# Optimization experiments

Measured on AMD Instinct MI355X. Metric: run time of the kernel, lower is better.

Reference implementation:

```python
import jax, jax.numpy as jnp
import numpy as np

N_HEAD = 16
MAX_SEQ_LEN = 2048
RATIO = 1
NEG_INF = -jnp.inf


def make_alibi_bias(n_head: int, max_seq_len: int, ratio: int) -> jnp.ndarray:
    # bias[t, s] = s*ratio - t, masked to -inf where > 0 (future positions)
    s = jnp.arange(max_seq_len)[None, :] * ratio            # [1, S]
    t = jnp.arange(max_seq_len * ratio)[:, None]            # [T, 1]
    bias = (s - t).astype(jnp.float32)                      # [T, S]
    bias = jnp.where(bias > 0, NEG_INF, bias)
    # per-head slopes: cumprod of 2^(-8/n_head) -> m_i = 2^(-8*(i+1)/n_head)
    m = jnp.cumprod(jnp.full((n_head,), 2.0 ** (-8.0 / n_head), dtype=jnp.float32))
    return bias[None, :, :] * m[:, None, None]              # [H, T, S]


def setup_inputs() -> dict:
    key = jax.random.key(0)
    kq, kk, kv = jax.random.split(key, 3)
    B, T, D = 2, 2048, 1024
    return {
        "q": jax.random.normal(kq, (B, T, D), dtype=jnp.float32),
        "k": jax.random.normal(kk, (B, T, D), dtype=jnp.float32),
        "v": jax.random.normal(kv, (B, T, D), dtype=jnp.float32),
    }


def reference(q, k, v):
    B, T, D = q.shape
    S = k.shape[1]
    H = N_HEAD
    dh = D // H
    # split heads: [B, T, D] -> [B, H, T, dh]
    qh = q.reshape(B, T, H, dh).transpose(0, 2, 1, 3)
    kh = k.reshape(B, S, H, dh).transpose(0, 2, 1, 3)
    vh = v.reshape(B, S, H, dh).transpose(0, 2, 1, 3)

    scores = jnp.einsum("bhtd,bhsd->bhts", qh, kh) / jnp.sqrt(jnp.float32(dh))
    bias = make_alibi_bias(H, MAX_SEQ_LEN, RATIO)[:, -T:, -S:]  # [H, T, S]
    attn = jax.nn.softmax(scores + bias[None], axis=-1)
    out = jnp.einsum("bhts,bhsd->bhtd", attn, vh)
    # gather heads: [B, H, T, dh] -> [B, T, D]
    return out.transpose(0, 2, 1, 3).reshape(B, T, D)
```

## Files before the change

### kernel.cpp

```cpp
#include <hip/hip_runtime.h>

#define N_HEAD 16
#define DHEAD 64
#define TSEQ 2048
#define DMODEL 1024
#define BATCH 2

typedef __bf16 bf16x8 __attribute__((ext_vector_type(8)));
typedef float f32x4 __attribute__((ext_vector_type(4)));

union BF8 { bf16x8 v; uint4 u; unsigned short us[8]; };

#if __has_builtin(__builtin_amdgcn_exp2f)
#define EXP2F(x) __builtin_amdgcn_exp2f(x)
#else
#define EXP2F(x) exp2f(x)
#endif

__device__ __forceinline__ unsigned short f2bf(float f) {
    unsigned u = __float_as_uint(f);
    u += 0x7fffu + ((u >> 16) & 1u);
    return (unsigned short)(u >> 16);
}

__device__ __forceinline__ bf16x8 load_bf8_f32(const float* p) {
    const float4 f0 = *(const float4*)p;
    const float4 f1 = *(const float4*)(p + 4);
    BF8 r;
    r.us[0] = f2bf(f0.x); r.us[1] = f2bf(f0.y);
    r.us[2] = f2bf(f0.z); r.us[3] = f2bf(f0.w);
    r.us[4] = f2bf(f1.x); r.us[5] = f2bf(f1.y);
    r.us[6] = f2bf(f1.z); r.us[7] = f2bf(f1.w);
    return r.v;
}

__global__ __launch_bounds__(256) void prep(const float* __restrict__ K,
                                            const float* __restrict__ V,
                                            unsigned short* __restrict__ Kp,
                                            unsigned short* __restrict__ Vt)
{
    __shared__ float tl[64][68];
    const int bh = blockIdx.y, b = bh >> 4, h = bh & 15;
    const int s0 = blockIdx.x * 64;
    const int t = threadIdx.x;
    const int r16 = t >> 4, c4 = (t & 15) * 4;
    #pragma unroll
    for (int pass = 0; pass < 4; ++pass) {
        const int row = pass * 16 + r16;
        const size_t goff = ((size_t)(b * TSEQ + s0 + row)) * DMODEL + h * DHEAD + c4;
        const float4 fk = *(const float4*)(K + goff);
        ushort4 ok;
        ok.x = f2bf(fk.x); ok.y = f2bf(fk.y); ok.z = f2bf(fk.z); ok.w = f2bf(fk.w);
        *(ushort4*)(Kp + (((size_t)bh * TSEQ + s0 + row) << 6) + c4) = ok;
        const float4 fv = *(const float4*)(V + goff);
        *(float4*)&tl[row][c4] = fv;
    }
    __syncthreads();
    const int d = t >> 2, sc = (t & 3) * 16;
    union { unsigned short us[8]; uint4 u; } pk0, pk1;
    #pragma unroll
    for (int j = 0; j < 8; ++j) pk0.us[j] = f2bf(tl[sc + j][d]);
    #pragma unroll
    for (int j = 0; j < 8; ++j) pk1.us[j] = f2bf(tl[sc + 8 + j][d]);
    unsigned short* vo = Vt + ((size_t)bh * DHEAD + d) * TSEQ + s0 + sc;
    *(uint4*)vo = pk0.u;
    *(uint4*)(vo + 8) = pk1.u;
}

struct KF { uint4 f[8]; };

__global__ __launch_bounds__(256, 2) void alibi_attn(
    const float* __restrict__ Q, const unsigned short* __restrict__ Kp,
    const unsigned short* __restrict__ Vt, float* __restrict__ O)
{
    __shared__ __align__(16) unsigned short p_lds[4][32][72];
    __shared__ __align__(16) float mlds[2][64][40];

    const int wave = threadIdx.x >> 6;
    const int lane = threadIdx.x & 63;
    const int quad = lane >> 4;
    const int l16  = lane & 15;
    const int rh   = wave & 1;
    const int par  = wave >> 1;

    const int bh = blockIdx.y;
    const int b  = bh >> 4;
    const int h  = bh & 15;

    const float LOG2E   = 1.44269504088896f;
    const float slope   = exp2f(-0.5f * (float)(h + 1));
    const float bslope2 = slope * LOG2E;
    const float sscale2 = 0.125f * LOG2E;
    const float step128 = 128.0f * bslope2;

    const float*          qp = Q  + (size_t)b * TSEQ * DMODEL + (size_t)h * DHEAD;
    const unsigned short* kp = Kp + (size_t)bh * TSEQ * DHEAD;
    const unsigned short* vp = Vt + (size_t)bh * DHEAD * TSEQ;

    const f32x4 zero4 = {0.f, 0.f, 0.f, 0.f};

    for (int half = 0; half < 2; ++half) {
        const int x   = half ? (31 - (int)blockIdx.x) : (int)blockIdx.x;
        const int q0b = x * 64;
        const int qrow_base = q0b + rh * 32;

        if (half) __syncthreads();

        bf16x8 aq[2][2];
        #pragma unroll
        for (int qs = 0; qs < 2; ++qs) {
            const float* qr = qp + (size_t)(qrow_base + qs * 16 + l16) * DMODEL + quad * 8;
            aq[qs][0] = load_bf8_f32(qr);
            aq[qs][1] = load_bf8_f32(qr + 32);
        }

        f32x4 o[2][4], lp[2], dd[2][4];
        #pragma unroll
        for (int qs = 0; qs < 2; ++qs) {
            lp[qs] = zero4;
            #pragma unroll
            for (int nt = 0; nt < 4; ++nt) o[qs][nt] = zero4;
        }
        const int kvs = 64 * par;
        #pragma unroll
        for (int qs = 0; qs < 2; ++qs)
            #pragma unroll
            for (int nt = 0; nt < 4; ++nt) {
                const int d0 = kvs + nt * 16 + l16 - (qrow_base + qs * 16 + quad * 4);
                f32x4 dv = {(float)d0, (float)(d0 - 1), (float)(d0 - 2), (float)(d0 - 3)};
                dd[qs][nt] = dv * bslope2;
            }

        auto loadK = [&](int t) {
            KF f;
            const unsigned short* kb = kp + ((size_t)(t * 64 + l16) << 6) + quad * 8;
            #pragma unroll
            for (int nt = 0; nt < 4; ++nt) {
                f.f[nt * 2 + 0] = *(const uint4*)(kb + nt * 1024);
                f.f[nt * 2 + 1] = *(const uint4*)(kb + nt * 1024 + 32);
            }
            return f;
        };

        auto compute = [&](const KF& kf, int t, bool masked) {
            const int kv0 = t * 64;
            uint4 vf[4][2];
            #pragma unroll
            for (int nt = 0; nt < 4; ++nt)
                #pragma unroll
                for (int ks = 0; ks < 2; ++ks)
                    vf[nt][ks] = *(const uint4*)(vp + (size_t)(nt * 16 + l16) * TSEQ +
                                                 kv0 + ks * 32 + quad * 8);
            f32x4 s[2][4];
            #pragma unroll
            for (int qs = 0; qs < 2; ++qs)
                #pragma unroll
                for (int nt = 0; nt < 4; ++nt) {
                    BF8 k0, k1;
                    k0.u = kf.f[nt * 2 + 0];
                    k1.u = kf.f[nt * 2 + 1];
                    f32x4 acc = zero4;
                    acc = __builtin_amdgcn_mfma_f32_16x16x32_bf16(aq[qs][0], k0.v, acc, 0, 0, 0);
                    acc = __builtin_amdgcn_mfma_f32_16x16x32_bf16(aq[qs][1], k1.v, acc, 0, 0, 0);
                    s[qs][nt] = acc;
                }
            #pragma unroll
            for (int qs = 0; qs < 2; ++qs)
                #pragma unroll
                for (int nt = 0; nt < 4; ++nt) {
                    f32x4 e = s[qs][nt] * sscale2 + dd[qs][nt];
                    f32x4 p;
                    if (!masked) {
                        #pragma unroll
                        for (int r = 0; r < 4; ++r) p[r] = EXP2F(e[r]);
                    } else {
                        const int db = kv0 + nt * 16 + l16 - (qrow_base + qs * 16 + quad * 4);
                        #pragma unroll
                        for (int r = 0; r < 4; ++r) {
                            const float v = EXP2F(e[r]);
                            p[r] = (db - r > 0) ? 0.f : v;
                        }
                    }
                    lp[qs] += p;
                    #pragma unroll
                    for (int r = 0; r < 4; ++r)
                        p_lds[wave][qs * 16 + quad * 4 + r][nt * 16 + l16] =
                            (unsigned short)(__float_as_uint(p[r]) >> 16);
                    dd[qs][nt] += step128;
                }
            asm volatile("s_waitcnt lgkmcnt(0)" ::: "memory");
            BF8 pa[2][2];
            #pragma unroll
            for (int qs = 0; qs < 2; ++qs)
                #pragma unroll
                for (int ks = 0; ks < 2; ++ks)
                    pa[qs][ks].u = *(const uint4*)&p_lds[wave][qs * 16 + l16][ks * 32 + quad * 8];
            #pragma unroll
            for (int qs = 0; qs < 2; ++qs)
                #pragma unroll
                for (int nt = 0; nt < 4; ++nt) {
                    BF8 v0, v1;
                    v0.u = vf[nt][0];
                    v1.u = vf[nt][1];
                    o[qs][nt] = __builtin_amdgcn_mfma_f32_16x16x32_bf16(pa[qs][0].v, v0.v, o[qs][nt], 0, 0, 0);
                    o[qs][nt] = __builtin_amdgcn_mfma_f32_16x16x32_bf16(pa[qs][1].v, v1.v, o[qs][nt], 0, 0, 0);
                }
        };

        if (par <= x) {
            int t = par;
            KF A = loadK(t);
            for (; t + 2 < x; t += 4) {
                KF B = loadK(t + 2);
                compute(A, t, false);
                const int tn = (t + 4 < x) ? (t + 4) : x;
                A = loadK(tn);
                compute(B, t + 2, false);
            }
            if (t == x) {
                compute(A, t, true);
            } else if (t == x - 1) {
                compute(A, t, false);
            } else if (t == x - 2) {
                KF B2 = loadK(x);
                compute(A, t, false);
                compute(B2, x, true);
            }
        }

        if (par == 1) {
            float* m = &mlds[rh][lane][0];
            #pragma unroll
            for (int qs = 0; qs < 2; ++qs)
                #pragma unroll
                for (int nt = 0; nt < 4; ++nt)
                    *(f32x4*)&m[(qs * 4 + nt) * 4] = o[qs][nt];
            *(f32x4*)&m[32] = lp[0];
            *(f32x4*)&m[36] = lp[1];
        }
        __syncthreads();
        if (par == 0) {
            const float* m = &mlds[rh][lane][0];
            #pragma unroll
            for (int qs = 0; qs < 2; ++qs)
                #pragma unroll
                for (int nt = 0; nt < 4; ++nt)
                    o[qs][nt] += *(const f32x4*)&m[(qs * 4 + nt) * 4];
            lp[0] += *(const f32x4*)&m[32];
            lp[1] += *(const f32x4*)&m[36];
            float ls[2][4];
            #pragma unroll
            for (int qs = 0; qs < 2; ++qs)
                #pragma unroll
                for (int r = 0; r < 4; ++r) {
                    float v = lp[qs][r];
                    v += __shfl_xor(v, 1);
                    v += __shfl_xor(v, 2);
                    v += __shfl_xor(v, 4);
                    v += __shfl_xor(v, 8);
                    ls[qs][r] = v;
                }
            #pragma unroll
            for (int qs = 0; qs < 2; ++qs)
                #pragma unroll
                for (int nt = 0; nt < 4; ++nt)
                    #pragma unroll
                    for (int r = 0; r < 4; ++r) {
                        const int trow = qrow_base + qs * 16 + quad * 4 + r;
                        O[((size_t)b * TSEQ + trow) * DMODEL + h * DHEAD + nt * 16 + l16] =
                            o[qs][nt][r] / ls[qs][r];
                    }
        }
    }
}

extern "C" void kernel_launch(void* const* d_in, const int* in_sizes, int n_in,
                              void* d_out, int out_size, void* d_ws, size_t ws_size,
                              hipStream_t stream) {
    const float* q = (const float*)d_in[0];
    const float* k = (const float*)d_in[1];
    const float* v = (const float*)d_in[2];
    float* out = (float*)d_out;

    unsigned short* Kp = (unsigned short*)d_ws;
    unsigned short* Vt = Kp + (size_t)BATCH * N_HEAD * TSEQ * DHEAD;

    prep<<<dim3(TSEQ / 64, BATCH * N_HEAD), 256, 0, stream>>>(k, v, Kp, Vt);
    alibi_attn<<<dim3(16, BATCH * N_HEAD), 256, 0, stream>>>(q, Kp, Vt, out);
}
```

Measured before the change: 157.1 us.

## Halve per-wave query rows, double grid, drop K prefetch pipeline

The attention kernel now gives each wave 16 query rows instead of 32, and each block covers 32-row tiles, so the grid doubles to 32x32 blocks with launch bounds raised to allow 4 blocks per CU. The explicit double-buffered K prefetch loop is replaced by a simple loop that loads K and V each iteration. The causal tile limit is computed per 16-row group, which trims some masked work. The aim is more occupancy and parallelism to hide latency, in exchange for less reuse of K/V per loaded tile and no software prefetch. The prep kernel also changes its LDS transpose padding from 68 to 65 and uses scalar stores.

Measured after the change: 211.4 us. 34.5% more time.

```diff
diff --git a/kernel.cpp b/kernel.cpp
--- a/kernel.cpp
+++ b/kernel.cpp
@@ -39,7 +39,7 @@
                                             unsigned short* __restrict__ Kp,
                                             unsigned short* __restrict__ Vt)
 {
-    __shared__ float tl[64][68];
+    __shared__ float tl[64][65];
     const int bh = blockIdx.y, b = bh >> 4, h = bh & 15;
     const int s0 = blockIdx.x * 64;
     const int t = threadIdx.x;
@@ -53,7 +53,8 @@
         ok.x = f2bf(fk.x); ok.y = f2bf(fk.y); ok.z = f2bf(fk.z); ok.w = f2bf(fk.w);
         *(ushort4*)(Kp + (((size_t)bh * TSEQ + s0 + row) << 6) + c4) = ok;
         const float4 fv = *(const float4*)(V + goff);
-        *(float4*)&tl[row][c4] = fv;
+        tl[row][c4 + 0] = fv.x; tl[row][c4 + 1] = fv.y;
+        tl[row][c4 + 2] = fv.z; tl[row][c4 + 3] = fv.w;
     }
     __syncthreads();
     const int d = t >> 2, sc = (t & 3) * 16;
@@ -67,14 +68,12 @@
     *(uint4*)(vo + 8) = pk1.u;
 }
 
-struct KF { uint4 f[8]; };
-
-__global__ __launch_bounds__(256, 2) void alibi_attn(
+__global__ __launch_bounds__(256, 4) void alibi_attn(
     const float* __restrict__ Q, const unsigned short* __restrict__ Kp,
     const unsigned short* __restrict__ Vt, float* __restrict__ O)
 {
-    __shared__ __align__(16) unsigned short p_lds[4][32][72];
-    __shared__ __align__(16) float mlds[2][64][40];
+    __shared__ __align__(16) unsigned short p_lds[4][16][72];
+    __shared__ __align__(16) float mlds[2][64][20];
 
     const int wave = threadIdx.x >> 6;
     const int lane = threadIdx.x & 63;
@@ -100,176 +99,119 @@
     const f32x4 zero4 = {0.f, 0.f, 0.f, 0.f};
 
     for (int half = 0; half < 2; ++half) {
-        const int x   = half ? (31 - (int)blockIdx.x) : (int)blockIdx.x;
-        const int q0b = x * 64;
-        const int qrow_base = q0b + rh * 32;
+        const int y    = half ? (63 - (int)blockIdx.x) : (int)blockIdx.x;
+        const int base = y * 32 + rh * 16;
+        const int amax = (base + 15) >> 6;
 
         if (half) __syncthreads();
 
-        bf16x8 aq[2][2];
+        const float* qr = qp + (size_t)(base + l16) * DMODEL + quad * 8;
+        const bf16x8 aq0 = load_bf8_f32(qr);
+        const bf16x8 aq1 = load_bf8_f32(qr + 32);
+
+        f32x4 o[4];
+        f32x4 lp = zero4;
         #pragma unroll
-        for (int qs = 0; qs < 2; ++qs) {
-            const float* qr = qp + (size_t)(qrow_base + qs * 16 + l16) * DMODEL + quad * 8;
-            aq[qs][0] = load_bf8_f32(qr);
-            aq[qs][1] = load_bf8_f32(qr + 32);
-        }
-
-        f32x4 o[2][4], lp[2], dd[2][4];
+        for (int nt = 0; nt < 4; ++nt) o[nt] = zero4;
+
+        float db[4];
         #pragma unroll
-        for (int qs = 0; qs < 2; ++qs) {
-            lp[qs] = zero4;
-            #pragma unroll
-            for (int nt = 0; nt < 4; ++nt) o[qs][nt] = zero4;
-        }
-        const int kvs = 64 * par;
-        #pragma unroll
-        for (int qs = 0; qs < 2; ++qs)
-            #pragma unroll
-            for (int nt = 0; nt < 4; ++nt) {
-                const int d0 = kvs + nt * 16 + l16 - (qrow_base + qs * 16 + quad * 4);
-                f32x4 dv = {(float)d0, (float)(d0 - 1), (float)(d0 - 2), (float)(d0 - 3)};
-                dd[qs][nt] = dv * bslope2;
-            }
-
-        auto loadK = [&](int t) {
-            KF f;
-            const unsigned short* kb = kp + ((size_t)(t * 64 + l16) << 6) + quad * 8;
-            #pragma unroll
-            for (int nt = 0; nt < 4; ++nt) {
-                f.f[nt * 2 + 0] = *(const uint4*)(kb + nt * 1024);
-                f.f[nt * 2 + 1] = *(const uint4*)(kb + nt * 1024 + 32);
-            }
-            return f;
-        };
-
-        auto compute = [&](const KF& kf, int t, bool masked) {
+        for (int nt = 0; nt < 4; ++nt)
+            db[nt] = (float)(64 * par + nt * 16 + l16 - base - quad * 4) * bslope2;
+
+        for (int t = par; t <= amax; t += 2) {
             const int kv0 = t * 64;
-            uint4 vf[4][2];
+            const unsigned short* kb = kp + ((size_t)(kv0 + l16) << 6) + quad * 8;
+            uint4 kf[8];
+            #pragma unroll
+            for (int nt = 0; nt < 4; ++nt) {
+                kf[nt * 2 + 0] = *(const uint4*)(kb + nt * 1024);
+                kf[nt * 2 + 1] = *(const uint4*)(kb + nt * 1024 + 32);
+            }
+            uint4 vf[8];
             #pragma unroll
             for (int nt = 0; nt < 4; ++nt)
                 #pragma unroll
                 for (int ks = 0; ks < 2; ++ks)
-                    vf[nt][ks] = *(const uint4*)(vp + (size_t)(nt * 16 + l16) * TSEQ +
-                                                 kv0 + ks * 32 + quad * 8);
-            f32x4 s[2][4];
-            #pragma unroll
-            for (int qs = 0; qs < 2; ++qs)
-                #pragma unroll
-                for (int nt = 0; nt < 4; ++nt) {
-                    BF8 k0, k1;
-                    k0.u = kf.f[nt * 2 + 0];
-                    k1.u = kf.f[nt * 2 + 1];
-                    f32x4 acc = zero4;
-                    acc = __builtin_amdgcn_mfma_f32_16x16x32_bf16(aq[qs][0], k0.v, acc, 0, 0, 0);
-                    acc = __builtin_amdgcn_mfma_f32_16x16x32_bf16(aq[qs][1], k1.v, acc, 0, 0, 0);
-                    s[qs][nt] = acc;
-                }
-            #pragma unroll
-            for (int qs = 0; qs < 2; ++qs)
-                #pragma unroll
-                for (int nt = 0; nt < 4; ++nt) {
-                    f32x4 e = s[qs][nt] * sscale2 + dd[qs][nt];
-                    f32x4 p;
-                    if (!masked) {
-                        #pragma unroll
-                        for (int r = 0; r < 4; ++r) p[r] = EXP2F(e[r]);
-                    } else {
-                        const int db = kv0 + nt * 16 + l16 - (qrow_base + qs * 16 + quad * 4);
-                        #pragma unroll
-                        for (int r = 0; r < 4; ++r) {
-                            const float v = EXP2F(e[r]);
-                            p[r] = (db - r > 0) ? 0.f : v;
-                        }
-                    }
-                    lp[qs] += p;
+                    vf[nt * 2 + ks] = *(const uint4*)(vp + (size_t)(nt * 16 + l16) * TSEQ +
+                                                      kv0 + ks * 32 + quad * 8);
+            f32x4 s[4];
+            #pragma unroll
+            for (int nt = 0; nt < 4; ++nt) {
+                BF8 k0, k1;
+                k0.u = kf[nt * 2 + 0];
+                k1.u = kf[nt * 2 + 1];
+                f32x4 acc = zero4;
+                acc = __builtin_amdgcn_mfma_f32_16x16x32_bf16(aq0, k0.v, acc, 0, 0, 0);
+                acc = __builtin_amdgcn_mfma_f32_16x16x32_bf16(aq1, k1.v, acc, 0, 0, 0);
+                s[nt] = acc;
+            }
+            const bool masked = (t == amax);
+            #pragma unroll
+            for (int nt = 0; nt < 4; ++nt) {
+                f32x4 p;
+                #pragma unroll
+                for (int r = 0; r < 4; ++r)
+                    p[r] = EXP2F(fmaf(s[nt][r], sscale2, db[nt] - (float)r * bslope2));
+                if (masked) {
+                    const int dbi = kv0 + nt * 16 + l16 - base - quad * 4;
                     #pragma unroll
                     for (int r = 0; r < 4; ++r)
-                        p_lds[wave][qs * 16 + quad * 4 + r][nt * 16 + l16] =
-                            (unsigned short)(__float_as_uint(p[r]) >> 16);
-                    dd[qs][nt] += step128;
+                        if (dbi - r > 0) p[r] = 0.f;
                 }
+                lp += p;
+                #pragma unroll
+                for (int r = 0; r < 4; ++r)
+                    p_lds[wave][quad * 4 + r][nt * 16 + l16] =
+                        (unsigned short)(__float_as_uint(p[r]) >> 16);
+                db[nt] += step128;
+            }
             asm volatile("s_waitcnt lgkmcnt(0)" ::: "memory");
-            BF8 pa[2][2];
-            #pragma unroll
-            for (int qs = 0; qs < 2; ++qs)
-                #pragma unroll
-                for (int ks = 0; ks < 2; ++ks)
-                    pa[qs][ks].u = *(const uint4*)&p_lds[wave][qs * 16 + l16][ks * 32 + quad * 8];
-            #pragma unroll
-            for (int qs = 0; qs < 2; ++qs)
-                #pragma unroll
-                for (int nt = 0; nt < 4; ++nt) {
-                    BF8 v0, v1;
-                    v0.u = vf[nt][0];
-                    v1.u = vf[nt][1];
-                    o[qs][nt] = __builtin_amdgcn_mfma_f32_16x16x32_bf16(pa[qs][0].v, v0.v, o[qs][nt], 0, 0, 0);
-                    o[qs][nt] = __builtin_amdgcn_mfma_f32_16x16x32_bf16(pa[qs][1].v, v1.v, o[qs][nt], 0, 0, 0);
-                }
-        };
-
-        if (par <= x) {
-            int t = par;
-            KF A = loadK(t);
-            for (; t + 2 < x; t += 4) {
-                KF B = loadK(t + 2);
-                compute(A, t, false);
-                const int tn = (t + 4 < x) ? (t + 4) : x;
-                A = loadK(tn);
-                compute(B, t + 2, false);
-            }
-            if (t == x) {
-                compute(A, t, true);
-            } else if (t == x - 1) {
-                compute(A, t, false);
-            } else if (t == x - 2) {
-                KF B2 = loadK(x);
-                compute(A, t, false);
-                compute(B2, x, true);
+            BF8 pa0, pa1;
+            pa0.u = *(const uint4*)&p_lds[wave][l16][quad * 8];
+            pa1.u = *(const uint4*)&p_lds[wave][l16][32 + quad * 8];
+            #pragma unroll
+            for (int nt = 0; nt < 4; ++nt) {
+                BF8 v0, v1;
+                v0.u = vf[nt * 2 + 0];
+                v1.u = vf[nt * 2 + 1];
+                o[nt] = __builtin_amdgcn_mfma_f32_16x16x32_bf16(pa0.v, v0.v, o[nt], 0, 0, 0);
+                o[nt] = __builtin_amdgcn_mfma_f32_16x16x32_bf16(pa1.v, v1.v, o[nt], 0, 0, 0);
             }
         }
 
         if (par == 1) {
             float* m = &mlds[rh][lane][0];
             #pragma unroll
-            for (int qs = 0; qs < 2; ++qs)
-                #pragma unroll
-                for (int nt = 0; nt < 4; ++nt)
-                    *(f32x4*)&m[(qs * 4 + nt) * 4] = o[qs][nt];
-            *(f32x4*)&m[32] = lp[0];
-            *(f32x4*)&m[36] = lp[1];
+            for (int nt = 0; nt < 4; ++nt)
+                *(f32x4*)&m[nt * 4] = o[nt];
+            *(f32x4*)&m[16] = lp;
         }
         __syncthreads();
         if (par == 0) {
             const float* m = &mlds[rh][lane][0];
             #pragma unroll
-            for (int qs = 0; qs < 2; ++qs)
-                #pragma unroll
-                for (int nt = 0; nt < 4; ++nt)
-                    o[qs][nt] += *(const f32x4*)&m[(qs * 4 + nt) * 4];
-            lp[0] += *(const f32x4*)&m[32];
-            lp[1] += *(const f32x4*)&m[36];
-            float ls[2][4];
-            #pragma unroll
-            for (int qs = 0; qs < 2; ++qs)
+            for (int nt = 0; nt < 4; ++nt)
+                o[nt] += *(const f32x4*)&m[nt * 4];
+            lp += *(const f32x4*)&m[16];
+            float ls[4];
+            #pragma unroll
+            for (int r = 0; r < 4; ++r) {
+                float v = lp[r];
+                v += __shfl_xor(v, 1);
+                v += __shfl_xor(v, 2);
+                v += __shfl_xor(v, 4);
+                v += __shfl_xor(v, 8);
+                ls[r] = v;
+            }
+            #pragma unroll
+            for (int nt = 0; nt < 4; ++nt)
                 #pragma unroll
                 for (int r = 0; r < 4; ++r) {
-                    float v = lp[qs][r];
-                    v += __shfl_xor(v, 1);
-                    v += __shfl_xor(v, 2);
-                    v += __shfl_xor(v, 4);
-                    v += __shfl_xor(v, 8);
-                    ls[qs][r] = v;
+                    const int trow = base + quad * 4 + r;
+                    O[((size_t)b * TSEQ + trow) * DMODEL + h * DHEAD + nt * 16 + l16] =
+                        o[nt][r] / ls[r];
                 }
-            #pragma unroll
-            for (int qs = 0; qs < 2; ++qs)
-                #pragma unroll
-                for (int nt = 0; nt < 4; ++nt)
-                    #pragma unroll
-                    for (int r = 0; r < 4; ++r) {
-                        const int trow = qrow_base + qs * 16 + quad * 4 + r;
-                        O[((size_t)b * TSEQ + trow) * DMODEL + h * DHEAD + nt * 16 + l16] =
-                            o[qs][nt][r] / ls[qs][r];
-                    }
         }
     }
 }
@@ -286,5 +228,5 @@
     unsigned short* Vt = Kp + (size_t)BATCH * N_HEAD * TSEQ * DHEAD;
 
     prep<<<dim3(TSEQ / 64, BATCH * N_HEAD), 256, 0, stream>>>(k, v, Kp, Vt);
-    alibi_attn<<<dim3(16, BATCH * N_HEAD), 256, 0, stream>>>(q, Kp, Vt, out);
-}
+    alibi_attn<<<dim3(32, BATCH * N_HEAD), 256, 0, stream>>>(q, Kp, Vt, out);
+}
```
